# Performance work log

Hardware: AMD Instinct MI355X
Metric: run time of the kernel (lower is better)

Reference implementation:

```python
import jax, jax.numpy as jnp
import numpy as np

NEG_SLOPE = 0.2  # PyG GATConv default negative_slope


def setup_inputs() -> dict:
    key = jax.random.key(0)
    k_x, k_e, k_w, k_as, k_ad = jax.random.split(key, 5)
    B, F, N, D, E, L = 2, 16, 5000, 128, 40000, 3
    x = jax.random.normal(k_x, (B, F, N, D), dtype=jnp.float32)
    edge_index = jax.random.randint(k_e, (B, F, 2, E), 0, N, dtype=jnp.int64)
    Ws = jax.random.normal(k_w, (L, D, D), dtype=jnp.float32) / np.float32(np.sqrt(D))
    att_src = jax.random.normal(k_as, (L, D), dtype=jnp.float32) / np.float32(np.sqrt(D))
    att_dst = jax.random.normal(k_ad, (L, D), dtype=jnp.float32) / np.float32(np.sqrt(D))
    bias = jnp.zeros((L, D), dtype=jnp.float32)
    return {"x": x, "edge_index": edge_index, "Ws": Ws,
            "att_src": att_src, "att_dst": att_dst, "bias": bias}


def _gat_layer(h, src, dst, n, W, a_s, a_d, b):
    # h: [n, D] node features; src/dst: [E_tot] edge endpoints (self-loops included)
    h2 = h @ W                                   # [n, D] transformed features
    s = h2 @ a_s                                 # [n] per-node source score
    d = h2 @ a_d                                 # [n] per-node dest score
    e = jax.nn.leaky_relu(s[src] + d[dst], NEG_SLOPE)   # [E_tot] raw attention
    m = jax.lax.stop_gradient(jax.ops.segment_max(e, dst, num_segments=n))
    ex = jnp.exp(e - m[dst])                     # numerically stable softmax per dst
    denom = jax.ops.segment_sum(ex, dst, num_segments=n)
    alpha = ex / denom[dst]                      # [E_tot] normalized attention
    out = jax.ops.segment_sum(alpha[:, None] * h2[src], dst, num_segments=n) + b
    return jax.nn.relu(out)


def reference(x, edge_index, Ws, att_src, att_dst, bias):
    B, F, N, D = x.shape
    n = B * F * N
    h = x.reshape(n, D)
    # faithful to torch: (BF,2,E).view(2,-1) is a raw row-major reshape
    ei = edge_index.reshape(2, -1)
    loop = jnp.arange(n, dtype=ei.dtype)         # PyG GATConv adds self-loops
    src = jnp.concatenate([ei[0], loop])
    dst = jnp.concatenate([ei[1], loop])
    for l in range(Ws.shape[0]):                 # fixed small layer loop
        h = _gat_layer(h, src, dst, n, Ws[l], att_src[l], att_dst[l], bias[l])
    return h.reshape(B, F, N, D)
```

## Files before the change

### kernel.cpp

```cpp
#include <hip/hip_runtime.h>
#include <math.h>

#define NODES_TOTAL 160000
#define NODES_REAL  5000
#define D 128
#define NEG 0.2f
#define KP2 128
#define HL2 (128 * KP2)
#define WT2_L (2 * HL2)

typedef unsigned short ushort_t;
typedef unsigned int uint_t;
typedef __attribute__((ext_vector_type(8))) __bf16 bf16x8;
typedef __attribute__((ext_vector_type(4))) float f32x4;
union BF8 { bf16x8 v; ushort_t u[8]; };

__device__ __forceinline__ void split2(float x, ushort_t& hi, ushort_t& lo) {
    unsigned u = __float_as_uint(x);
    hi = (ushort_t)(u >> 16);
    float hif = __uint_as_float(u & 0xffff0000u);
    lo = (ushort_t)(__float_as_uint(x - hif) >> 16);
}
__device__ __forceinline__ uint_t encmax(float f) {
    uint_t b = __float_as_uint(f);
    return b ^ ((uint_t)((int)b >> 31) | 0x80000000u);
}
__device__ __forceinline__ float decmax(uint_t u) {
    uint_t b = (u & 0x80000000u) ? (u ^ 0x80000000u) : ~u;
    return __uint_as_float(b);
}

__global__ void zero_kernel(int* counts, uint_t* gmaxu) {
    int i = blockIdx.x * blockDim.x + threadIdx.x;
    if (i < NODES_REAL) counts[i] = 0;
    if (i < 3) gmaxu[i] = 0u;
}

__global__ void rank_kernel(const int* __restrict__ ei, int* __restrict__ counts,
                            ushort_t* __restrict__ rank16, int Eh) {
    int e = blockIdx.x * blockDim.x + threadIdx.x;
    if (e < Eh) {
        int d = ei[Eh + e];
        int r = atomicAdd(&counts[d], 1);
        rank16[e] = (ushort_t)r;
    }
}

__global__ void scan_kernel(const int* __restrict__ counts, int* __restrict__ offs) {
    __shared__ int sd[1024];
    int t = threadIdx.x;
    int pre[5]; int sum = 0;
    #pragma unroll
    for (int u = 0; u < 5; ++u) {
        int idx = t * 5 + u;
        int c = (idx < NODES_REAL) ? counts[idx] : 0;
        pre[u] = sum; sum += c;
    }
    sd[t] = sum;
    __syncthreads();
    int run = sum;
    for (int o = 1; o < 1024; o <<= 1) {
        int v = (t >= o) ? sd[t - o] : 0;
        __syncthreads();
        sd[t] += v;
        __syncthreads();
    }
    int excl = sd[t] - run;
    #pragma unroll
    for (int u = 0; u < 5; ++u) {
        int idx = t * 5 + u;
        if (idx < NODES_REAL) offs[idx] = excl + pre[u];
    }
    if (t == 1023) offs[NODES_REAL] = excl + run;
}

__global__ void scatter_det(const int* __restrict__ ei, const int* __restrict__ offs,
                            const ushort_t* __restrict__ rank16, ushort_t* __restrict__ esrc,
                            int Eh) {
    int e = blockIdx.x * blockDim.x + threadIdx.x;
    if (e < Eh) {
        int s = ei[e];
        int d = ei[Eh + e];
        esrc[offs[d] + (int)rank16[e]] = (ushort_t)s;
    }
}

__global__ void wsplit_kernel(const float* __restrict__ Ws, ushort_t* __restrict__ Wt,
                              ushort_t* __restrict__ Wm) {
    int l  = blockIdx.x >> 3;
    int n  = (blockIdx.x & 7) * 16 + (threadIdx.x >> 4);
    int c8 = threadIdx.x & 15;
    int k0 = c8 * 8;
    const float* src = Ws + (size_t)l * D * D;
    union { ushort_t u[8]; uint4 v; } hi, lo;
    #pragma unroll
    for (int j = 0; j < 8; ++j) split2(src[(size_t)(k0 + j) * D + n], hi.u[j], lo.u[j]);
    int c8s = c8 ^ (n & 15);
    ushort_t* dhi = Wt + (size_t)l * WT2_L + n * KP2 + c8s * 8;
    *(uint4*)dhi = hi.v;
    *(uint4*)(dhi + HL2) = lo.v;
    int ct = n >> 4, m16 = n & 15, kc = c8 >> 2, qq = c8 & 3;
    int lane = qq * 16 + m16;
    ushort_t* d2 = Wm + (size_t)l * WT2_L + ((ct * 4 + kc) * 2 + 0) * 512 + lane * 8;
    *(uint4*)d2 = hi.v;
    *(uint4*)(d2 + 512) = lo.v;
}

__global__ __launch_bounds__(256, 2)
void mlp3_kernel(const float* __restrict__ x, const ushort_t* __restrict__ Wm,
                 const float* __restrict__ bs, float* __restrict__ out) {
    __shared__ float scr[2][2][16][132];
    int tid = threadIdx.x;
    int w = tid >> 6, lane = tid & 63, q = lane >> 4, m16 = lane & 15;
    int p = w >> 1, h = w & 1;
    int row0 = NODES_REAL + blockIdx.x * 64 + p * 32;

    float4 xa[2][4][2];
    #pragma unroll
    for (int rt = 0; rt < 2; ++rt) {
        int r = row0 + rt * 16 + m16;
        if (r > NODES_TOTAL - 1) r = NODES_TOTAL - 1;
        #pragma unroll
        for (int kc = 0; kc < 4; ++kc) {
            const float* gp = x + (size_t)r * D + kc * 32 + q * 8;
            xa[rt][kc][0] = *(const float4*)gp;
            xa[rt][kc][1] = *(const float4*)(gp + 4);
        }
    }

    f32x4 acc[2][4];
    #pragma unroll
    for (int l = 0; l < 3; ++l) {
        const ushort_t* Wml = Wm + (size_t)l * WT2_L;
        if (l > 0) __syncthreads();

        BF8 ahi[2][4], alo[2][4];
        #pragma unroll
        for (int rt = 0; rt < 2; ++rt)
            #pragma unroll
            for (int kc = 0; kc < 4; ++kc) {
                float4 v0, v1;
                if (l == 0) { v0 = xa[rt][kc][0]; v1 = xa[rt][kc][1]; }
                else {
                    const float* sp = &scr[p][rt][m16][kc * 32 + q * 8];
                    v0 = *(const float4*)sp; v1 = *(const float4*)(sp + 4);
                }
                float xv[8] = {v0.x, v0.y, v0.z, v0.w, v1.x, v1.y, v1.z, v1.w};
                #pragma unroll
                for (int j = 0; j < 8; ++j) split2(xv[j], ahi[rt][kc].u[j], alo[rt][kc].u[j]);
            }
        if (l > 0) __syncthreads();

        #pragma unroll
        for (int rt = 0; rt < 2; ++rt)
            #pragma unroll
            for (int ct = 0; ct < 4; ++ct) acc[rt][ct] = (f32x4){0.f, 0.f, 0.f, 0.f};

        #pragma unroll
        for (int ph = 0; ph < 2; ++ph) {
            int kc0 = ph * 2;
            bf16x8 bh[4][2], bl[4][2];
            #pragma unroll
            for (int ct = 0; ct < 4; ++ct)
                #pragma unroll
                for (int dk = 0; dk < 2; ++dk) {
                    const ushort_t* bp = Wml + (((h * 4 + ct) * 4 + (kc0 + dk)) * 2) * 512 + lane * 8;
                    bh[ct][dk] = *(const bf16x8*)bp;
                    bl[ct][dk] = *(const bf16x8*)(bp + 512);
                }
            #pragma unroll
            for (int dk = 0; dk < 2; ++dk)
                #pragma unroll
                for (int ct = 0; ct < 4; ++ct)
                    #pragma unroll
                    for (int rt = 0; rt < 2; ++rt) {
                        acc[rt][ct] = __builtin_amdgcn_mfma_f32_16x16x32_bf16(ahi[rt][kc0 + dk].v, bh[ct][dk], acc[rt][ct], 0, 0, 0);
                        acc[rt][ct] = __builtin_amdgcn_mfma_f32_16x16x32_bf16(ahi[rt][kc0 + dk].v, bl[ct][dk], acc[rt][ct], 0, 0, 0);
                        acc[rt][ct] = __builtin_amdgcn_mfma_f32_16x16x32_bf16(alo[rt][kc0 + dk].v, bh[ct][dk], acc[rt][ct], 0, 0, 0);
                    }
        }
        float bv[4];
        #pragma unroll
        for (int ct = 0; ct < 4; ++ct) bv[ct] = bs[l * D + (h * 4 + ct) * 16 + m16];
        #pragma unroll
        for (int rt = 0; rt < 2; ++rt)
            #pragma unroll
            for (int ct = 0; ct < 4; ++ct)
                #pragma unroll
                for (int reg = 0; reg < 4; ++reg)
                    scr[p][rt][q * 4 + reg][(h * 4 + ct) * 16 + m16] =
                        fmaxf(acc[rt][ct][reg] + bv[ct], 0.f);
    }
    __syncthreads();
    #pragma unroll
    for (int i = 0; i < 8; ++i) {
        int rowl = i * 2 + (lane >> 5);
        int grow = row0 + h * 16 + rowl;
        float4 v = *(const float4*)&scr[p][h][rowl][(lane & 31) * 4];
        if (grow < NODES_TOTAL)
            *(float4*)&out[(size_t)grow * D + (lane & 31) * 4] = v;
    }
}

__global__ __launch_bounds__(256)
void gsmall_kernel(const float* __restrict__ hin, const ushort_t* __restrict__ Wlg,
                   const float* __restrict__ a_s, const float* __restrict__ a_d,
                   float* __restrict__ h2, float* __restrict__ sv, float* __restrict__ dv,
                   uint_t* __restrict__ gmaxu) {
    __shared__ ushort_t Wl[WT2_L];
    int tid = threadIdx.x;
    {
        const uint4* gw = (const uint4*)Wlg;
        uint4* lw = (uint4*)Wl;
        #pragma unroll
        for (int r = 0; r < 16; ++r) lw[r * 256 + tid] = gw[r * 256 + tid];
    }
    int w = tid >> 6, lane = tid & 63, q = lane >> 4, m16 = lane & 15;
    int row0 = blockIdx.x * 128 + w * 32;
    f32x4 acc[2][8];
    #pragma unroll
    for (int rt = 0; rt < 2; ++rt)
        #pragma unroll
        for (int ct = 0; ct < 8; ++ct) acc[rt][ct] = (f32x4){0.f, 0.f, 0.f, 0.f};
    float4 xa[2][4][2];
    #pragma unroll
    for (int rt = 0; rt < 2; ++rt) {
        int r = row0 + rt * 16 + m16;
        if (r > NODES_REAL - 1) r = NODES_REAL - 1;
        #pragma unroll
        for (int kc = 0; kc < 4; ++kc) {
            const float* gp = hin + (size_t)r * D + kc * 32 + q * 8;
            xa[rt][kc][0] = *(const float4*)gp;
            xa[rt][kc][1] = *(const float4*)(gp + 4);
        }
    }
    __syncthreads();
    #pragma unroll
    for (int kc = 0; kc < 4; ++kc) {
        BF8 ahi[2], alo[2];
        #pragma unroll
        for (int rt = 0; rt < 2; ++rt) {
            float4 v0 = xa[rt][kc][0], v1 = xa[rt][kc][1];
            float xv[8] = {v0.x, v0.y, v0.z, v0.w, v1.x, v1.y, v1.z, v1.w};
            #pragma unroll
            for (int j = 0; j < 8; ++j) split2(xv[j], ahi[rt].u[j], alo[rt].u[j]);
        }
        #pragma unroll
        for (int ct = 0; ct < 8; ++ct) {
            const ushort_t* bp = Wl + (ct * 16 + m16) * KP2 + (((kc * 4 + q) ^ m16) * 8);
            bf16x8 bhi = *(const bf16x8*)bp;
            bf16x8 blo = *(const bf16x8*)(bp + HL2);
            #pragma unroll
            for (int rt = 0; rt < 2; ++rt) {
                acc[rt][ct] = __builtin_amdgcn_mfma_f32_16x16x32_bf16(ahi[rt].v, bhi, acc[rt][ct], 0, 0, 0);
                acc[rt][ct] = __builtin_amdgcn_mfma_f32_16x16x32_bf16(ahi[rt].v, blo, acc[rt][ct], 0, 0, 0);
                acc[rt][ct] = __builtin_amdgcn_mfma_f32_16x16x32_bf16(alo[rt].v, bhi, acc[rt][ct], 0, 0, 0);
            }
        }
    }
    #pragma unroll
    for (int rt = 0; rt < 2; ++rt)
        #pragma unroll
        for (int reg = 0; reg < 4; ++reg) {
            int grow = row0 + rt * 16 + q * 4 + reg;
            if (grow < NODES_REAL) {
                #pragma unroll
                for (int ct = 0; ct < 8; ++ct)
                    h2[(size_t)grow * D + ct * 16 + m16] = acc[rt][ct][reg];
            }
        }
    float asv[8], adv[8];
    #pragma unroll
    for (int ct = 0; ct < 8; ++ct) { asv[ct] = a_s[ct * 16 + m16]; adv[ct] = a_d[ct * 16 + m16]; }
    #pragma unroll
    for (int rt = 0; rt < 2; ++rt)
        #pragma unroll
        for (int reg = 0; reg < 4; ++reg) {
            float ps = 0.f, pd = 0.f;
            #pragma unroll
            for (int ct = 0; ct < 8; ++ct) {
                float v = acc[rt][ct][reg];
                ps += v * asv[ct]; pd += v * adv[ct];
            }
            #pragma unroll
            for (int o = 1; o < 16; o <<= 1) { ps += __shfl_xor(ps, o); pd += __shfl_xor(pd, o); }
            int grow = row0 + rt * 16 + q * 4 + reg;
            if (m16 == 0 && grow < NODES_REAL) {
                sv[grow] = ps; dv[grow] = pd;
                atomicMax(gmaxu, encmax(ps));
            }
        }
}

__global__ __launch_bounds__(256)
void agg_kernel(const float* __restrict__ h2, const float* __restrict__ sv,
                const float* __restrict__ dv, const int* __restrict__ offs,
                const ushort_t* __restrict__ esrc, const float* __restrict__ bias,
                float* __restrict__ out, const uint_t* __restrict__ gmaxu) {
    int w = threadIdx.x >> 6, lane = threadIdx.x & 63;
    int i = blockIdx.x * 4 + w;
    int start = offs[i], end = offs[i + 1];
    float d_i = dv[i];
    float gm = decmax(*gmaxu) + d_i;
    float m = gm > 0.f ? gm : NEG * gm;
    float ax = 0.f, ay = 0.f, ax1 = 0.f, ay1 = 0.f, exs = 0.f;
    for (int base = start; base < end; base += 64) {
        int cnt = min(64, end - base);
        int srci = (lane < cnt) ? (int)esrc[base + lane] : 0;
        float sc = sv[srci] + d_i;
        sc = sc > 0.f ? sc : NEG * sc;
        float ex = (lane < cnt) ? __expf(sc - m) : 0.f;
        exs += ex;
        if (cnt == 64) {
            #pragma unroll 4
            for (int j = 0; j < 64; j += 2) {
                int   s0 = __shfl(srci, j),     s1 = __shfl(srci, j + 1);
                float e0 = __shfl(ex, j),       e1 = __shfl(ex, j + 1);
                float2 h0 = *(const float2*)&h2[(size_t)s0 * D + 2 * lane];
                float2 h1 = *(const float2*)&h2[(size_t)s1 * D + 2 * lane];
                ax  += e0 * h0.x; ay  += e0 * h0.y;
                ax1 += e1 * h1.x; ay1 += e1 * h1.y;
            }
        } else {
            for (int j = 0; j < cnt; ++j) {
                int   src = __shfl(srci, j);
                float e   = __shfl(ex, j);
                float2 hv = *(const float2*)&h2[(size_t)src * D + 2 * lane];
                ax += e * hv.x; ay += e * hv.y;
            }
        }
    }
    ax += ax1; ay += ay1;
    float scf = sv[i] + d_i; scf = scf > 0.f ? scf : NEG * scf;
    float exf = __expf(scf - m);
    float2 hv = *(const float2*)&h2[(size_t)i * D + 2 * lane];
    ax += exf * hv.x; ay += exf * hv.y;
    #pragma unroll
    for (int o = 1; o < 64; o <<= 1) exs += __shfl_xor(exs, o);
    float rd = 1.f / (exs + exf);
    float2 b2 = *(const float2*)&bias[2 * lane];
    float2 o2 = make_float2(fmaxf(ax * rd + b2.x, 0.f), fmaxf(ay * rd + b2.y, 0.f));
    *(float2*)&out[(size_t)i * D + 2 * lane] = o2;
}

extern "C" void kernel_launch(void* const* d_in, const int* in_sizes, int n_in,
                              void* d_out, int out_size, void* d_ws, size_t ws_size,
                              hipStream_t stream) {
    const float* x   = (const float*)d_in[0];
    const int*   ei  = (const int*)d_in[1];
    const float* Ws  = (const float*)d_in[2];
    const float* as_ = (const float*)d_in[3];
    const float* ad_ = (const float*)d_in[4];
    const float* bs  = (const float*)d_in[5];
    float* out = (float*)d_out;
    int Eh = in_sizes[1] / 2;

    char* ws = (char*)d_ws;
    float*    h2     = (float*)ws;
    float*    bufS   = (float*)(ws + 2560000);
    float*    sv     = (float*)(ws + 5120000);
    float*    dv     = (float*)(ws + 5140000);
    int*      counts = (int*)  (ws + 5160000);
    int*      offs   = (int*)  (ws + 5180000);
    ushort_t* rank16 = (ushort_t*)(ws + 5200016);
    ushort_t* esrc   = (ushort_t*)(ws + 7760016);
    ushort_t* Wt     = (ushort_t*)(ws + 10320016);
    uint_t*   gmaxu  = (uint_t*)(ws + 10528912);
    ushort_t* Wm     = (ushort_t*)(ws + 10528928);

    zero_kernel<<<(NODES_REAL + 255) / 256, 256, 0, stream>>>(counts, gmaxu);
    rank_kernel<<<(Eh + 255) / 256, 256, 0, stream>>>(ei, counts, rank16, Eh);
    scan_kernel<<<1, 1024, 0, stream>>>(counts, offs);
    scatter_det<<<(Eh + 255) / 256, 256, 0, stream>>>(ei, offs, rank16, esrc, Eh);
    wsplit_kernel<<<24, 256, 0, stream>>>(Ws, Wt, Wm);

    mlp3_kernel<<<(NODES_TOTAL - NODES_REAL + 63) / 64, 256, 0, stream>>>(x, Wm, bs, out);

    for (int l = 0; l < 3; ++l) {
        const float* hin = (l == 0) ? x : bufS;
        float* hout = (l == 2) ? out : bufS;
        gsmall_kernel<<<(NODES_REAL + 127) / 128, 256, 0, stream>>>(
            hin, Wt + (size_t)l * WT2_L, as_ + l * D, ad_ + l * D, h2, sv, dv, gmaxu + l);
        agg_kernel<<<(NODES_REAL + 3) / 4, 256, 0, stream>>>(
            h2, sv, dv, offs, esrc, bs + l * D, hout, gmaxu + l);
    }
}
```

Before: 513.0 us.

## Shrink GEMM blocks, read MFMA-layout weights from global, widen aggregation unroll

The isolated-node MLP kernel now runs 128-thread blocks over 32 rows each, so there are twice as many blocks and less shared memory per block. The small-graph GEMM drops its 64KB shared-memory weight staging and loads B fragments straight from global in MFMA-ready layout, using one wave per 16 rows. This spreads its 313 blocks across many CUs instead of 40 blocks. The Wt buffer and its write in wsplit are removed, and the aggregation loop keeps four independent accumulators to have more gathers in flight. The cost is repeated global or L2 weight reads per wave, plus some register pressure from the wider unroll.

```diff
diff --git a/kernel.cpp b/kernel.cpp
--- a/kernel.cpp
+++ b/kernel.cpp
@@ -85,8 +85,7 @@
     }
 }
 
-__global__ void wsplit_kernel(const float* __restrict__ Ws, ushort_t* __restrict__ Wt,
-                              ushort_t* __restrict__ Wm) {
+__global__ void wsplit_kernel(const float* __restrict__ Ws, ushort_t* __restrict__ Wm) {
     int l  = blockIdx.x >> 3;
     int n  = (blockIdx.x & 7) * 16 + (threadIdx.x >> 4);
     int c8 = threadIdx.x & 15;
@@ -95,10 +94,6 @@
     union { ushort_t u[8]; uint4 v; } hi, lo;
     #pragma unroll
     for (int j = 0; j < 8; ++j) split2(src[(size_t)(k0 + j) * D + n], hi.u[j], lo.u[j]);
-    int c8s = c8 ^ (n & 15);
-    ushort_t* dhi = Wt + (size_t)l * WT2_L + n * KP2 + c8s * 8;
-    *(uint4*)dhi = hi.v;
-    *(uint4*)(dhi + HL2) = lo.v;
     int ct = n >> 4, m16 = n & 15, kc = c8 >> 2, qq = c8 & 3;
     int lane = qq * 16 + m16;
     ushort_t* d2 = Wm + (size_t)l * WT2_L + ((ct * 4 + kc) * 2 + 0) * 512 + lane * 8;
@@ -106,14 +101,13 @@
     *(uint4*)(d2 + 512) = lo.v;
 }
 
-__global__ __launch_bounds__(256, 2)
+__global__ __launch_bounds__(128, 4)
 void mlp3_kernel(const float* __restrict__ x, const ushort_t* __restrict__ Wm,
                  const float* __restrict__ bs, float* __restrict__ out) {
-    __shared__ float scr[2][2][16][132];
+    __shared__ float scr[2][16][132];
     int tid = threadIdx.x;
-    int w = tid >> 6, lane = tid & 63, q = lane >> 4, m16 = lane & 15;
-    int p = w >> 1, h = w & 1;
-    int row0 = NODES_REAL + blockIdx.x * 64 + p * 32;
+    int h = tid >> 6, lane = tid & 63, q = lane >> 4, m16 = lane & 15;
+    int row0 = NODES_REAL + blockIdx.x * 32;
 
     float4 xa[2][4][2];
     #pragma unroll
@@ -142,7 +136,7 @@
                 float4 v0, v1;
                 if (l == 0) { v0 = xa[rt][kc][0]; v1 = xa[rt][kc][1]; }
                 else {
-                    const float* sp = &scr[p][rt][m16][kc * 32 + q * 8];
+                    const float* sp = &scr[rt][m16][kc * 32 + q * 8];
                     v0 = *(const float4*)sp; v1 = *(const float4*)(sp + 4);
                 }
                 float xv[8] = {v0.x, v0.y, v0.z, v0.w, v1.x, v1.y, v1.z, v1.w};
@@ -188,7 +182,7 @@
             for (int ct = 0; ct < 4; ++ct)
                 #pragma unroll
                 for (int reg = 0; reg < 4; ++reg)
-                    scr[p][rt][q * 4 + reg][(h * 4 + ct) * 16 + m16] =
+                    scr[rt][q * 4 + reg][(h * 4 + ct) * 16 + m16] =
                         fmaxf(acc[rt][ct][reg] + bv[ct], 0.f);
     }
     __syncthreads();
@@ -196,100 +190,85 @@
     for (int i = 0; i < 8; ++i) {
         int rowl = i * 2 + (lane >> 5);
         int grow = row0 + h * 16 + rowl;
-        float4 v = *(const float4*)&scr[p][h][rowl][(lane & 31) * 4];
+        float4 v = *(const float4*)&scr[h][rowl][(lane & 31) * 4];
         if (grow < NODES_TOTAL)
             *(float4*)&out[(size_t)grow * D + (lane & 31) * 4] = v;
     }
 }
 
-__global__ __launch_bounds__(256)
-void gsmall_kernel(const float* __restrict__ hin, const ushort_t* __restrict__ Wlg,
+__global__ __launch_bounds__(64, 2)
+void gsmall_kernel(const float* __restrict__ hin, const ushort_t* __restrict__ Wm,
                    const float* __restrict__ a_s, const float* __restrict__ a_d,
                    float* __restrict__ h2, float* __restrict__ sv, float* __restrict__ dv,
                    uint_t* __restrict__ gmaxu) {
-    __shared__ ushort_t Wl[WT2_L];
-    int tid = threadIdx.x;
+    int lane = threadIdx.x & 63, q = lane >> 4, m16 = lane & 15;
+    int row0 = blockIdx.x * 16;
+    float4 xa[4][2];
     {
-        const uint4* gw = (const uint4*)Wlg;
-        uint4* lw = (uint4*)Wl;
-        #pragma unroll
-        for (int r = 0; r < 16; ++r) lw[r * 256 + tid] = gw[r * 256 + tid];
-    }
-    int w = tid >> 6, lane = tid & 63, q = lane >> 4, m16 = lane & 15;
-    int row0 = blockIdx.x * 128 + w * 32;
-    f32x4 acc[2][8];
-    #pragma unroll
-    for (int rt = 0; rt < 2; ++rt)
-        #pragma unroll
-        for (int ct = 0; ct < 8; ++ct) acc[rt][ct] = (f32x4){0.f, 0.f, 0.f, 0.f};
-    float4 xa[2][4][2];
-    #pragma unroll
-    for (int rt = 0; rt < 2; ++rt) {
-        int r = row0 + rt * 16 + m16;
+        int r = row0 + m16;
         if (r > NODES_REAL - 1) r = NODES_REAL - 1;
         #pragma unroll
         for (int kc = 0; kc < 4; ++kc) {
             const float* gp = hin + (size_t)r * D + kc * 32 + q * 8;
-            xa[rt][kc][0] = *(const float4*)gp;
-            xa[rt][kc][1] = *(const float4*)(gp + 4);
-        }
-    }
-    __syncthreads();
+            xa[kc][0] = *(const float4*)gp;
+            xa[kc][1] = *(const float4*)(gp + 4);
+        }
+    }
+    f32x4 acc[8];
+    #pragma unroll
+    for (int ct = 0; ct < 8; ++ct) acc[ct] = (f32x4){0.f, 0.f, 0.f, 0.f};
+
     #pragma unroll
     for (int kc = 0; kc < 4; ++kc) {
-        BF8 ahi[2], alo[2];
-        #pragma unroll
-        for (int rt = 0; rt < 2; ++rt) {
-            float4 v0 = xa[rt][kc][0], v1 = xa[rt][kc][1];
+        BF8 ahi, alo;
+        {
+            float4 v0 = xa[kc][0], v1 = xa[kc][1];
             float xv[8] = {v0.x, v0.y, v0.z, v0.w, v1.x, v1.y, v1.z, v1.w};
             #pragma unroll
-            for (int j = 0; j < 8; ++j) split2(xv[j], ahi[rt].u[j], alo[rt].u[j]);
-        }
+            for (int j = 0; j < 8; ++j) split2(xv[j], ahi.u[j], alo.u[j]);
+        }
+        bf16x8 bh[8], bl[8];
         #pragma unroll
         for (int ct = 0; ct < 8; ++ct) {
-            const ushort_t* bp = Wl + (ct * 16 + m16) * KP2 + (((kc * 4 + q) ^ m16) * 8);
-            bf16x8 bhi = *(const bf16x8*)bp;
-            bf16x8 blo = *(const bf16x8*)(bp + HL2);
-            #pragma unroll
-            for (int rt = 0; rt < 2; ++rt) {
-                acc[rt][ct] = __builtin_amdgcn_mfma_f32_16x16x32_bf16(ahi[rt].v, bhi, acc[rt][ct], 0, 0, 0);
-                acc[rt][ct] = __builtin_amdgcn_mfma_f32_16x16x32_bf16(ahi[rt].v, blo, acc[rt][ct], 0, 0, 0);
-                acc[rt][ct] = __builtin_amdgcn_mfma_f32_16x16x32_bf16(alo[rt].v, bhi, acc[rt][ct], 0, 0, 0);
-            }
-        }
-    }
-    #pragma unroll
-    for (int rt = 0; rt < 2; ++rt)
-        #pragma unroll
-        for (int reg = 0; reg < 4; ++reg) {
-            int grow = row0 + rt * 16 + q * 4 + reg;
-            if (grow < NODES_REAL) {
-                #pragma unroll
-                for (int ct = 0; ct < 8; ++ct)
-                    h2[(size_t)grow * D + ct * 16 + m16] = acc[rt][ct][reg];
-            }
-        }
+            const ushort_t* bp = Wm + ((ct * 4 + kc) * 2) * 512 + lane * 8;
+            bh[ct] = *(const bf16x8*)bp;
+            bl[ct] = *(const bf16x8*)(bp + 512);
+        }
+        #pragma unroll
+        for (int ct = 0; ct < 8; ++ct) {
+            acc[ct] = __builtin_amdgcn_mfma_f32_16x16x32_bf16(ahi.v, bh[ct], acc[ct], 0, 0, 0);
+            acc[ct] = __builtin_amdgcn_mfma_f32_16x16x32_bf16(ahi.v, bl[ct], acc[ct], 0, 0, 0);
+            acc[ct] = __builtin_amdgcn_mfma_f32_16x16x32_bf16(alo.v, bh[ct], acc[ct], 0, 0, 0);
+        }
+    }
+    #pragma unroll
+    for (int reg = 0; reg < 4; ++reg) {
+        int grow = row0 + q * 4 + reg;
+        if (grow < NODES_REAL) {
+            #pragma unroll
+            for (int ct = 0; ct < 8; ++ct)
+                h2[(size_t)grow * D + ct * 16 + m16] = acc[ct][reg];
+        }
+    }
     float asv[8], adv[8];
     #pragma unroll
     for (int ct = 0; ct < 8; ++ct) { asv[ct] = a_s[ct * 16 + m16]; adv[ct] = a_d[ct * 16 + m16]; }
     #pragma unroll
-    for (int rt = 0; rt < 2; ++rt)
-        #pragma unroll
-        for (int reg = 0; reg < 4; ++reg) {
-            float ps = 0.f, pd = 0.f;
-            #pragma unroll
-            for (int ct = 0; ct < 8; ++ct) {
-                float v = acc[rt][ct][reg];
-                ps += v * asv[ct]; pd += v * adv[ct];
-            }
-            #pragma unroll
-            for (int o = 1; o < 16; o <<= 1) { ps += __shfl_xor(ps, o); pd += __shfl_xor(pd, o); }
-            int grow = row0 + rt * 16 + q * 4 + reg;
-            if (m16 == 0 && grow < NODES_REAL) {
-                sv[grow] = ps; dv[grow] = pd;
-                atomicMax(gmaxu, encmax(ps));
-            }
-        }
+    for (int reg = 0; reg < 4; ++reg) {
+        float ps = 0.f, pd = 0.f;
+        #pragma unroll
+        for (int ct = 0; ct < 8; ++ct) {
+            float v = acc[ct][reg];
+            ps += v * asv[ct]; pd += v * adv[ct];
+        }
+        #pragma unroll
+        for (int o = 1; o < 16; o <<= 1) { ps += __shfl_xor(ps, o); pd += __shfl_xor(pd, o); }
+        int grow = row0 + q * 4 + reg;
+        if (m16 == 0 && grow < NODES_REAL) {
+            sv[grow] = ps; dv[grow] = pd;
+            atomicMax(gmaxu, encmax(ps));
+        }
+    }
 }
 
 __global__ __launch_bounds__(256)
@@ -303,7 +282,9 @@
     float d_i = dv[i];
     float gm = decmax(*gmaxu) + d_i;
     float m = gm > 0.f ? gm : NEG * gm;
-    float ax = 0.f, ay = 0.f, ax1 = 0.f, ay1 = 0.f, exs = 0.f;
+    const float2* h2v = (const float2*)h2;
+    float ax0 = 0.f, ay0 = 0.f, ax1 = 0.f, ay1 = 0.f;
+    float ax2 = 0.f, ay2 = 0.f, ax3 = 0.f, ay3 = 0.f, exs = 0.f;
     for (int base = start; base < end; base += 64) {
         int cnt = min(64, end - base);
         int srci = (lane < cnt) ? (int)esrc[base + lane] : 0;
@@ -312,28 +293,35 @@
         float ex = (lane < cnt) ? __expf(sc - m) : 0.f;
         exs += ex;
         if (cnt == 64) {
-            #pragma unroll 4
-            for (int j = 0; j < 64; j += 2) {
+            #pragma unroll 2
+            for (int j = 0; j < 64; j += 4) {
                 int   s0 = __shfl(srci, j),     s1 = __shfl(srci, j + 1);
+                int   s2 = __shfl(srci, j + 2), s3 = __shfl(srci, j + 3);
                 float e0 = __shfl(ex, j),       e1 = __shfl(ex, j + 1);
-                float2 h0 = *(const float2*)&h2[(size_t)s0 * D + 2 * lane];
-                float2 h1 = *(const float2*)&h2[(size_t)s1 * D + 2 * lane];
-                ax  += e0 * h0.x; ay  += e0 * h0.y;
-                ax1 += e1 * h1.x; ay1 += e1 * h1.y;
+                float e2 = __shfl(ex, j + 2),   e3 = __shfl(ex, j + 3);
+                float2 hv0 = h2v[(size_t)s0 * 64 + lane];
+                float2 hv1 = h2v[(size_t)s1 * 64 + lane];
+                float2 hv2 = h2v[(size_t)s2 * 64 + lane];
+                float2 hv3 = h2v[(size_t)s3 * 64 + lane];
+                ax0 += e0 * hv0.x; ay0 += e0 * hv0.y;
+                ax1 += e1 * hv1.x; ay1 += e1 * hv1.y;
+                ax2 += e2 * hv2.x; ay2 += e2 * hv2.y;
+                ax3 += e3 * hv3.x; ay3 += e3 * hv3.y;
             }
         } else {
             for (int j = 0; j < cnt; ++j) {
                 int   src = __shfl(srci, j);
                 float e   = __shfl(ex, j);
-                float2 hv = *(const float2*)&h2[(size_t)src * D + 2 * lane];
-                ax += e * hv.x; ay += e * hv.y;
+                float2 hv = h2v[(size_t)src * 64 + lane];
+                ax0 += e * hv.x; ay0 += e * hv.y;
             }
         }
     }
-    ax += ax1; ay += ay1;
+    float ax = (ax0 + ax1) + (ax2 + ax3);
+    float ay = (ay0 + ay1) + (ay2 + ay3);
     float scf = sv[i] + d_i; scf = scf > 0.f ? scf : NEG * scf;
     float exf = __expf(scf - m);
-    float2 hv = *(const float2*)&h2[(size_t)i * D + 2 * lane];
+    float2 hv = h2v[(size_t)i * 64 + lane];
     ax += exf * hv.x; ay += exf * hv.y;
     #pragma unroll
     for (int o = 1; o < 64; o <<= 1) exs += __shfl_xor(exs, o);
@@ -364,23 +352,22 @@
     int*      offs   = (int*)  (ws + 5180000);
     ushort_t* rank16 = (ushort_t*)(ws + 5200016);
     ushort_t* esrc   = (ushort_t*)(ws + 7760016);
-    ushort_t* Wt     = (ushort_t*)(ws + 10320016);
+    ushort_t* Wm     = (ushort_t*)(ws + 10320016);
     uint_t*   gmaxu  = (uint_t*)(ws + 10528912);
-    ushort_t* Wm     = (ushort_t*)(ws + 10528928);
 
     zero_kernel<<<(NODES_REAL + 255) / 256, 256, 0, stream>>>(counts, gmaxu);
     rank_kernel<<<(Eh + 255) / 256, 256, 0, stream>>>(ei, counts, rank16, Eh);
     scan_kernel<<<1, 1024, 0, stream>>>(counts, offs);
     scatter_det<<<(Eh + 255) / 256, 256, 0, stream>>>(ei, offs, rank16, esrc, Eh);
-    wsplit_kernel<<<24, 256, 0, stream>>>(Ws, Wt, Wm);
-
-    mlp3_kernel<<<(NODES_TOTAL - NODES_REAL + 63) / 64, 256, 0, stream>>>(x, Wm, bs, out);
+    wsplit_kernel<<<24, 256, 0, stream>>>(Ws, Wm);
+
+    mlp3_kernel<<<(NODES_TOTAL - NODES_REAL + 31) / 32, 128, 0, stream>>>(x, Wm, bs, out);
 
     for (int l = 0; l < 3; ++l) {
         const float* hin = (l == 0) ? x : bufS;
         float* hout = (l == 2) ? out : bufS;
-        gsmall_kernel<<<(NODES_REAL + 127) / 128, 256, 0, stream>>>(
-            hin, Wt + (size_t)l * WT2_L, as_ + l * D, ad_ + l * D, h2, sv, dv, gmaxu + l);
+        gsmall_kernel<<<(NODES_REAL + 15) / 16, 64, 0, stream>>>(
+            hin, Wm + (size_t)l * WT2_L, as_ + l * D, ad_ + l * D, h2, sv, dv, gmaxu + l);
         agg_kernel<<<(NODES_REAL + 3) / 4, 256, 0, stream>>>(
             h2, sv, dv, offs, esrc, bs + l * D, hout, gmaxu + l);
     }
```

After: 566.4 us. +10.4%, slower.
